# Kernel optimization log

Hardware: AMD Instinct MI355X
Metric: run time of the kernel (lower is better)

The kernel has to match this reference:

```python
import jax, jax.numpy as jnp
import numpy as np

STATE_LEN = 128
SEQ_LEN = 2048  # middle segment length; total T = SEQ_LEN + 2*STATE_LEN = 2304


def _l2norm(t):
    # matches torch F.normalize(p=2, dim=-1, eps=1e-12)
    n = jnp.sqrt(jnp.sum(t * t, axis=-1, keepdims=True))
    return t / jnp.maximum(n, 1e-12)


def setup_inputs() -> dict:
    key = jax.random.key(0)
    ks = jax.random.split(key, 8)
    B, D, H, dk, dv = 1, 1024, 16, 64, 64
    T = SEQ_LEN + 2 * STATE_LEN
    x = jax.random.normal(ks[0], (B, T, D), dtype=jnp.float32)
    w = lambda k, do: jax.random.normal(k, (H, D, do), dtype=jnp.float32) * 0.02
    return {
        "x": x,
        "Wq": w(ks[1], dk),
        "Wk": w(ks[2], dk),
        "Wv": w(ks[3], dv),
        "Wq_state": w(ks[4], dk),
        "Wk_state": w(ks[5], dk),
        "Wv_state": w(ks[6], dv),
        "scaling_factor": jnp.full((H,), 1.0 / np.sqrt(dk), dtype=jnp.float32),
    }


def reference(x, Wq, Wk, Wv, Wq_state, Wk_state, Wv_state, scaling_factor):
    sl, seq = STATE_LEN, SEQ_LEN
    # extract_state: [start_state | sequence | end_state]
    x0 = x[:, :sl]
    xm = x[:, sl:sl + seq]
    x1 = x[:, sl + seq:]

    proj = lambda t, W: jnp.einsum('bsd,hdk->bhsk', t, W)  # StackedLinear, no bias

    q = jnp.concatenate([_l2norm(proj(x0, Wq_state)), _l2norm(proj(xm, Wq)), _l2norm(proj(x1, Wq_state))], axis=2)
    k = jnp.concatenate([_l2norm(proj(x0, Wk_state)), _l2norm(proj(xm, Wk)), _l2norm(proj(x1, Wk_state))], axis=2)
    v = jnp.concatenate([_l2norm(proj(x0, Wv_state)), _l2norm(proj(xm, Wv)), _l2norm(proj(x1, Wv_state))], axis=2)

    T = q.shape[2]
    row = jnp.arange(T)[:, None]
    col = jnp.arange(T)[None, :]
    allowed = col <= row  # causal (tril, diagonal=0)
    # end-state rows may not attend to start-state cols (attn_bias[..., seq+sl:seq+2sl, :sl] = 0 before log)
    allowed = allowed & ~((row >= sl + seq) & (col < sl))
    mask = jnp.where(allowed, 0.0, -jnp.inf).astype(q.dtype)  # log of 0/1 tril

    # per-head learnable scale applied to q@k^T, then additive mask, softmax, @v
    scores = jnp.einsum('bhqd,bhkd->bhqk', q, k) * scaling_factor[None, :, None, None] + mask
    att = jax.nn.softmax(scores, axis=-1)
    return jnp.einsum('bhqk,bhkd->bhqd', att, v)
```

## Files before the change

kernel.cpp:

```cpp
#include <hip/hip_runtime.h>
#include <hip/hip_bf16.h>

#define T_TOT 2304
#define DDIM  1024
#define NH    16
#define DK    64
#define SLEN  128
#define SEQ   2048

typedef __bf16 bf16x8 __attribute__((ext_vector_type(8)));
typedef __bf16 bf16x4 __attribute__((ext_vector_type(4)));
typedef float  f32x4  __attribute__((ext_vector_type(4)));

__device__ __forceinline__ void async_copy16(const void* gsrc, void* ldst) {
  __builtin_amdgcn_global_load_lds(
      (const __attribute__((address_space(1))) void*)gsrc,
      (__attribute__((address_space(3))) void*)ldst, 16, 0, 0);
}

__global__ __launch_bounds__(256) void convert_kernel(
    const float* __restrict__ x,
    const float* __restrict__ Wq, const float* __restrict__ Wk,
    const float* __restrict__ Wv, const float* __restrict__ Wqs,
    const float* __restrict__ Wks, const float* __restrict__ Wvs,
    __bf16* __restrict__ xb, __bf16* __restrict__ Wt) {
  const int b = blockIdx.x;
  const int tid = threadIdx.x;
  if (b < 576) {
    const float4* xin = (const float4*)x;
#pragma unroll
    for (int it = 0; it < 4; ++it) {
      int idx4 = b * 1024 + it * 256 + tid;
      float4 v = xin[idx4];
      bf16x4 o;
      o[0] = (__bf16)v.x; o[1] = (__bf16)v.y; o[2] = (__bf16)v.z; o[3] = (__bf16)v.w;
      *(bf16x4*)(xb + (size_t)idx4 * 4) = o;
    }
    return;
  }
  __shared__ float tile[64 * 65];
  const int wb = b - 576;
  const int m  = wb >> 8;
  const int rem = wb & 255;
  const int h  = rem >> 4;
  const int dt = rem & 15;
  const int d0 = dt * 64;
  const float* Wsrc = (m == 0 ? Wq : m == 1 ? Wk : m == 2 ? Wv
                      : m == 3 ? Wqs : m == 4 ? Wks : Wvs) + (size_t)h * (DDIM * DK);
#pragma unroll
  for (int rr = 0; rr < 4; ++rr) {
    int drow = rr * 16 + (tid >> 4);
    int nc   = (tid & 15) * 4;
    float4 v = *(const float4*)(Wsrc + (size_t)(d0 + drow) * DK + nc);
    tile[(nc + 0) * 65 + drow] = v.x;
    tile[(nc + 1) * 65 + drow] = v.y;
    tile[(nc + 2) * 65 + drow] = v.z;
    tile[(nc + 3) * 65 + drow] = v.w;
  }
  __syncthreads();
  {
    int n  = tid >> 2;
    int rg = (tid & 3) * 16;
    __bf16* dst = Wt + (((size_t)(m * NH + h)) * DK + n) * DDIM + d0 + rg;
    bf16x8 o0, o1;
#pragma unroll
    for (int e = 0; e < 8; e++) o0[e] = (__bf16)tile[n * 65 + rg + e];
#pragma unroll
    for (int e = 0; e < 8; e++) o1[e] = (__bf16)tile[n * 65 + rg + 8 + e];
    *(bf16x8*)dst = o0;
    *(bf16x8*)(dst + 8) = o1;
  }
}

__global__ __launch_bounds__(256) void proj_kernel(
    const __bf16* __restrict__ xb, const __bf16* __restrict__ Wt,
    const float* __restrict__ scal,
    __bf16* __restrict__ qkv, __bf16* __restrict__ vt) {
  const int ntile = blockIdx.x;
  const int rt    = blockIdx.y;
  const int which = blockIdx.z;
  const int r0    = rt * 128;
  const int m     = (rt == 0 || rt == 17) ? which + 3 : which;

  __shared__ __bf16 Xs[128 * 64];
  __shared__ __bf16 Wsh[128 * 64];

  const int tid  = threadIdx.x;
  const int wave = tid >> 6, lane = tid & 63;
  const int quad = lane >> 4, lc = lane & 15;
  const int wr   = wave >> 1, wc = wave & 1;
  const int h    = ntile * 2 + wc;

  const __bf16* Wbase = Wt + ((size_t)m * NH) * (DK * DDIM) + (size_t)(ntile * 128) * DDIM;

  const f32x4 fz = {0.f, 0.f, 0.f, 0.f};
  f32x4 acc[4][4];
#pragma unroll
  for (int i = 0; i < 4; i++)
#pragma unroll
    for (int j = 0; j < 4; j++) acc[i][j] = fz;

  for (int k0 = 0; k0 < DDIM; k0 += 64) {
#pragma unroll
    for (int it = 0; it < 4; ++it) {
      int L = it * 256 + tid;
      int row = L >> 3, c = (L & 7) ^ ((L >> 3) & 7);
      async_copy16(xb + (size_t)(r0 + row) * DDIM + k0 + c * 8,
                   (char*)Xs + (size_t)(it * 256 + wave * 64) * 16);
    }
#pragma unroll
    for (int it = 0; it < 4; ++it) {
      int L = it * 256 + tid;
      int row = L >> 3, c = (L & 7) ^ ((L >> 3) & 7);
      async_copy16(Wbase + (size_t)row * DDIM + k0 + c * 8,
                   (char*)Wsh + (size_t)(it * 256 + wave * 64) * 16);
    }
    __syncthreads();
#pragma unroll
    for (int kk = 0; kk < 2; kk++) {
      bf16x8 afr[4], bfr[4];
#pragma unroll
      for (int i = 0; i < 4; i++) {
        int row = wr * 64 + i * 16 + lc;
        int ch  = (kk * 4 + quad) ^ (row & 7);
        afr[i] = *(const bf16x8*)(Xs + (row * 8 + ch) * 8);
      }
#pragma unroll
      for (int j = 0; j < 4; j++) {
        int row = wc * 64 + j * 16 + lc;
        int ch  = (kk * 4 + quad) ^ (row & 7);
        bfr[j] = *(const bf16x8*)(Wsh + (row * 8 + ch) * 8);
      }
#pragma unroll
      for (int i = 0; i < 4; i++)
#pragma unroll
        for (int j = 0; j < 4; j++)
          acc[i][j] = __builtin_amdgcn_mfma_f32_16x16x32_bf16(afr[i], bfr[j], acc[i][j], 0, 0, 0);
    }
    __syncthreads();
  }

  const float qscale = (which == 0) ? scal[h] : 1.0f;
  float inv4[4][4];
#pragma unroll
  for (int i = 0; i < 4; i++) {
#pragma unroll
    for (int r = 0; r < 4; r++) {
      float s = 0.f;
#pragma unroll
      for (int j = 0; j < 4; j++) { float v = acc[i][j][r]; s += v * v; }
#pragma unroll
      for (int off = 1; off < 16; off <<= 1) s += __shfl_xor(s, off, 64);
      inv4[i][r] = qscale / fmaxf(sqrtf(s), 1e-12f);
    }
  }
  if (which == 2) {
    __bf16* vtp = vt + (size_t)h * (DK * T_TOT);
#pragma unroll
    for (int i = 0; i < 4; i++) {
      int rowbase = r0 + wr * 64 + i * 16 + quad * 4;
#pragma unroll
      for (int j = 0; j < 4; j++) {
        bf16x4 o;
#pragma unroll
        for (int r = 0; r < 4; r++) o[r] = (__bf16)(acc[i][j][r] * inv4[i][r]);
        *(bf16x4*)(vtp + (size_t)(j * 16 + lc) * T_TOT + rowbase) = o;
      }
    }
  } else {
    __bf16* outp = qkv + ((size_t)(which * NH + h)) * ((size_t)T_TOT * DK);
#pragma unroll
    for (int i = 0; i < 4; i++)
#pragma unroll
      for (int r = 0; r < 4; r++) {
        int row = r0 + wr * 64 + i * 16 + quad * 4 + r;
#pragma unroll
        for (int j = 0; j < 4; j++)
          outp[(size_t)row * DK + j * 16 + lc] = (__bf16)(acc[i][j][r] * inv4[i][r]);
      }
  }
}

__global__ __launch_bounds__(256) void attn_kernel(
    const __bf16* __restrict__ qkv, const __bf16* __restrict__ vt,
    float* __restrict__ out) {
  const int b    = blockIdx.x;
  const int h    = b & 15;
  const int qg   = 35 - (b >> 4);
  const int q0b  = qg * 64;
  const int tid  = threadIdx.x;
  const int wave = tid >> 6, lane = tid & 63;
  const int quad = lane >> 4, lc = lane & 15;
  const int q0w  = q0b + wave * 16;

  const __bf16* qp = qkv + ((size_t)h) * ((size_t)T_TOT * DK);
  const __bf16* kp = qkv + ((size_t)(NH + h)) * ((size_t)T_TOT * DK);
  const __bf16* vp = vt + (size_t)h * (DK * T_TOT);

  __shared__ __bf16 Ks[2][64 * 64];
  __shared__ __bf16 Vs[2][64 * 64];
  __shared__ __bf16 Ps[4][16 * 64];

  bf16x8 qf[2];
#pragma unroll
  for (int kk = 0; kk < 2; kk++)
    qf[kk] = *(const bf16x8*)(qp + (size_t)(q0w + lc) * DK + kk * 32 + quad * 8);

  const f32x4 fz = {0.f, 0.f, 0.f, 0.f};
  f32x4 acc_o[4];
#pragma unroll
  for (int ct = 0; ct < 4; ct++) acc_o[ct] = fz;
  float m_i = -__builtin_inff(), l_i = 0.f;

  const int jstart = (q0b >= SLEN + SEQ) ? 2 : 0;
  const int jend   = qg;

  auto stage = [&](int j, int bufi) {
    const __bf16* kT = kp + (size_t)j * 64 * DK;
#pragma unroll
    for (int it = 0; it < 2; ++it) {
      int L = it * 256 + tid;
      int row = L >> 3, c = (L & 7) ^ (L >> 3 & 7);
      async_copy16(kT + row * DK + c * 8,
                   (char*)&Ks[bufi][0] + (size_t)(it * 256 + wave * 64) * 16);
    }
#pragma unroll
    for (int it = 0; it < 2; ++it) {
      int L = it * 256 + tid;
      int row = L >> 3, c = (L & 7) ^ (L >> 3 & 7);
      async_copy16(vp + (size_t)row * T_TOT + j * 64 + c * 8,
                   (char*)&Vs[bufi][0] + (size_t)(it * 256 + wave * 64) * 16);
    }
  };

  stage(jstart, 0);
  int cur = 0;

  for (int j = jstart; j <= jend; ++j) {
    __syncthreads();
    if (j < jend) stage(j + 1, cur ^ 1);

    const int c0 = j * 64;
    const bool diag = (j == jend);

    f32x4 s[4];
#pragma unroll
    for (int ct = 0; ct < 4; ct++) {
      s[ct] = fz;
#pragma unroll
      for (int kk = 0; kk < 2; kk++) {
        int row = ct * 16 + lc;
        bf16x8 kA = *(const bf16x8*)(&Ks[cur][(row * 8 + (((kk * 4 + quad)) ^ (row & 7))) * 8]);
        s[ct] = __builtin_amdgcn_mfma_f32_16x16x32_bf16(kA, qf[kk], s[ct], 0, 0, 0);
      }
    }

    float mx = -__builtin_inff();
#pragma unroll
    for (int ct = 0; ct < 4; ct++)
#pragma unroll
      for (int r = 0; r < 4; r++) {
        float v = s[ct][r];
        if (diag && (c0 + ct * 16 + quad * 4 + r) > (q0w + lc)) v = -__builtin_inff();
        s[ct][r] = v;
        mx = fmaxf(mx, v);
      }
    mx = fmaxf(mx, __shfl_xor(mx, 16, 64));
    mx = fmaxf(mx, __shfl_xor(mx, 32, 64));
    float mnew  = fmaxf(m_i, mx);
    float alpha = __expf(m_i - mnew);
    float rs = 0.f;
#pragma unroll
    for (int ct = 0; ct < 4; ct++)
#pragma unroll
      for (int r = 0; r < 4; r++) {
        float pe = __expf(s[ct][r] - mnew);
        s[ct][r] = pe;
        rs += pe;
      }
    rs += __shfl_xor(rs, 16, 64);
    rs += __shfl_xor(rs, 32, 64);
    l_i = l_i * alpha + rs;
    m_i = mnew;
#pragma unroll
    for (int ct = 0; ct < 4; ct++)
#pragma unroll
      for (int r = 0; r < 4; r++) acc_o[ct][r] *= alpha;

#pragma unroll
    for (int ct = 0; ct < 4; ct++) {
      bf16x4 pb;
#pragma unroll
      for (int r = 0; r < 4; r++) pb[r] = (__bf16)s[ct][r];
      int cc = ct * 2 + (quad >> 1);
      int el = lc * 64 + ((cc ^ (lc & 7)) * 8) + (quad & 1) * 4;
      *(bf16x4*)(&Ps[wave][el]) = pb;
    }

#pragma unroll
    for (int kq = 0; kq < 2; kq++) {
      int cc = kq * 4 + quad;
      bf16x8 pB = *(const bf16x8*)(&Ps[wave][lc * 64 + ((cc ^ (lc & 7)) * 8)]);
#pragma unroll
      for (int ct = 0; ct < 4; ct++) {
        int vrow = ct * 16 + lc;
        bf16x8 vA = *(const bf16x8*)(&Vs[cur][(vrow * 8 + ((cc) ^ (vrow & 7))) * 8]);
        acc_o[ct] = __builtin_amdgcn_mfma_f32_16x16x32_bf16(vA, pB, acc_o[ct], 0, 0, 0);
      }
    }
    cur ^= 1;
  }

  float invl = 1.0f / l_i;
#pragma unroll
  for (int ct = 0; ct < 4; ct++) {
    f32x4 o;
#pragma unroll
    for (int r = 0; r < 4; r++) o[r] = acc_o[ct][r] * invl;
    *(f32x4*)(&out[((size_t)h * T_TOT + q0w + lc) * DK + ct * 16 + quad * 4]) = o;
  }
}

extern "C" void kernel_launch(void* const* d_in, const int* in_sizes, int n_in,
                              void* d_out, int out_size, void* d_ws, size_t ws_size,
                              hipStream_t stream) {
  const float* x    = (const float*)d_in[0];
  const float* Wq   = (const float*)d_in[1];
  const float* Wk   = (const float*)d_in[2];
  const float* Wv   = (const float*)d_in[3];
  const float* Wqs  = (const float*)d_in[4];
  const float* Wks  = (const float*)d_in[5];
  const float* Wvs  = (const float*)d_in[6];
  const float* scal = (const float*)d_in[7];
  float* out = (float*)d_out;

  char* ws = (char*)d_ws;
  size_t off = 0;
  __bf16* xb  = (__bf16*)(ws + off); off += (size_t)T_TOT * DDIM * 2;
  __bf16* Wt  = (__bf16*)(ws + off); off += (size_t)6 * NH * DK * DDIM * 2;
  __bf16* qkv = (__bf16*)(ws + off); off += (size_t)2 * NH * T_TOT * DK * 2;
  __bf16* vt  = (__bf16*)(ws + off);

  convert_kernel<<<2112, 256, 0, stream>>>(x, Wq, Wk, Wv, Wqs, Wks, Wvs, xb, Wt);
  proj_kernel<<<dim3(8, 18, 3), 256, 0, stream>>>(xb, Wt, scal, qkv, vt);
  attn_kernel<<<dim3(576), 256, 0, stream>>>(qkv, vt, out);
}
```

Before: 163.8 us.

## Use 128-wide KV tiles in attention and fold log2e into query scale

The attention loop now stages 128-key K and V tiles per iteration instead of 64, with a 16-chunk XOR swizzle for V and P. This halves the number of loop iterations and barriers per query block, and on the diagonal tile it skips the MFMAs that would be fully masked. The query scale is premultiplied by log2(e) so the softmax can use exp2f in place of __expf. Shared memory per block doubles and register pressure rises, which may reduce occupancy.

```diff
diff --git a/kernel.cpp b/kernel.cpp
--- a/kernel.cpp
+++ b/kernel.cpp
@@ -140,7 +140,7 @@
     __syncthreads();
   }
 
-  const float qscale = (which == 0) ? scal[h] : 1.0f;
+  const float qscale = (which == 0) ? scal[h] * 1.44269504088896f : 1.0f;
   float inv4[4][4];
 #pragma unroll
   for (int i = 0; i < 4; i++) {
@@ -197,9 +197,9 @@
   const __bf16* kp = qkv + ((size_t)(NH + h)) * ((size_t)T_TOT * DK);
   const __bf16* vp = vt + (size_t)h * (DK * T_TOT);
 
-  __shared__ __bf16 Ks[2][64 * 64];
-  __shared__ __bf16 Vs[2][64 * 64];
-  __shared__ __bf16 Ps[4][16 * 64];
+  __shared__ __bf16 Ks[2][128 * 64];
+  __shared__ __bf16 Vs[2][64 * 128];
+  __shared__ __bf16 Ps[4][16 * 128];
 
   bf16x8 qf[2];
 #pragma unroll
@@ -212,23 +212,23 @@
   for (int ct = 0; ct < 4; ct++) acc_o[ct] = fz;
   float m_i = -__builtin_inff(), l_i = 0.f;
 
-  const int jstart = (q0b >= SLEN + SEQ) ? 2 : 0;
-  const int jend   = qg;
+  const int jstart = (q0b >= SLEN + SEQ) ? 1 : 0;
+  const int jend   = q0b >> 7;
 
   auto stage = [&](int j, int bufi) {
-    const __bf16* kT = kp + (size_t)j * 64 * DK;
-#pragma unroll
-    for (int it = 0; it < 2; ++it) {
+    const __bf16* kT = kp + (size_t)j * 128 * DK;
+#pragma unroll
+    for (int it = 0; it < 4; ++it) {
       int L = it * 256 + tid;
-      int row = L >> 3, c = (L & 7) ^ (L >> 3 & 7);
+      int row = L >> 3, c = (L & 7) ^ ((L >> 3) & 7);
       async_copy16(kT + row * DK + c * 8,
                    (char*)&Ks[bufi][0] + (size_t)(it * 256 + wave * 64) * 16);
     }
 #pragma unroll
-    for (int it = 0; it < 2; ++it) {
+    for (int it = 0; it < 4; ++it) {
       int L = it * 256 + tid;
-      int row = L >> 3, c = (L & 7) ^ (L >> 3 & 7);
-      async_copy16(vp + (size_t)row * T_TOT + j * 64 + c * 8,
+      int d = L >> 4, c = (L & 15) ^ ((L >> 4) & 15);
+      async_copy16(vp + (size_t)d * T_TOT + j * 128 + c * 8,
                    (char*)&Vs[bufi][0] + (size_t)(it * 256 + wave * 64) * 16);
     }
   };
@@ -240,44 +240,58 @@
     __syncthreads();
     if (j < jend) stage(j + 1, cur ^ 1);
 
-    const int c0 = j * 64;
+    const int c0 = j * 128;
     const bool diag = (j == jend);
-
-    f32x4 s[4];
-#pragma unroll
-    for (int ct = 0; ct < 4; ct++) {
+    const int ctmax = diag ? ((q0b & 64) ? 7 : 3) : 7;
+
+    f32x4 s[8];
+#pragma unroll
+    for (int ct = 0; ct < 8; ct++) {
       s[ct] = fz;
-#pragma unroll
-      for (int kk = 0; kk < 2; kk++) {
-        int row = ct * 16 + lc;
-        bf16x8 kA = *(const bf16x8*)(&Ks[cur][(row * 8 + (((kk * 4 + quad)) ^ (row & 7))) * 8]);
-        s[ct] = __builtin_amdgcn_mfma_f32_16x16x32_bf16(kA, qf[kk], s[ct], 0, 0, 0);
+      if (ct <= ctmax) {
+#pragma unroll
+        for (int kk = 0; kk < 2; kk++) {
+          int row = ct * 16 + lc;
+          bf16x8 kA = *(const bf16x8*)(&Ks[cur][(row * 8 + ((kk * 4 + quad) ^ (row & 7))) * 8]);
+          s[ct] = __builtin_amdgcn_mfma_f32_16x16x32_bf16(kA, qf[kk], s[ct], 0, 0, 0);
+        }
       }
     }
 
     float mx = -__builtin_inff();
-#pragma unroll
-    for (int ct = 0; ct < 4; ct++)
-#pragma unroll
-      for (int r = 0; r < 4; r++) {
-        float v = s[ct][r];
-        if (diag && (c0 + ct * 16 + quad * 4 + r) > (q0w + lc)) v = -__builtin_inff();
-        s[ct][r] = v;
-        mx = fmaxf(mx, v);
-      }
+    if (diag) {
+#pragma unroll
+      for (int ct = 0; ct < 8; ct++) {
+        if (ct > ctmax) break;
+#pragma unroll
+        for (int r = 0; r < 4; r++) {
+          float v = s[ct][r];
+          if ((c0 + ct * 16 + quad * 4 + r) > (q0w + lc)) v = -__builtin_inff();
+          s[ct][r] = v;
+          mx = fmaxf(mx, v);
+        }
+      }
+    } else {
+#pragma unroll
+      for (int ct = 0; ct < 8; ct++)
+#pragma unroll
+        for (int r = 0; r < 4; r++) mx = fmaxf(mx, s[ct][r]);
+    }
     mx = fmaxf(mx, __shfl_xor(mx, 16, 64));
     mx = fmaxf(mx, __shfl_xor(mx, 32, 64));
     float mnew  = fmaxf(m_i, mx);
-    float alpha = __expf(m_i - mnew);
+    float alpha = exp2f(m_i - mnew);
     float rs = 0.f;
 #pragma unroll
-    for (int ct = 0; ct < 4; ct++)
+    for (int ct = 0; ct < 8; ct++) {
+      if (ct > ctmax) break;
 #pragma unroll
       for (int r = 0; r < 4; r++) {
-        float pe = __expf(s[ct][r] - mnew);
+        float pe = exp2f(s[ct][r] - mnew);
         s[ct][r] = pe;
         rs += pe;
       }
+    }
     rs += __shfl_xor(rs, 16, 64);
     rs += __shfl_xor(rs, 32, 64);
     l_i = l_i * alpha + rs;
@@ -288,23 +302,26 @@
       for (int r = 0; r < 4; r++) acc_o[ct][r] *= alpha;
 
 #pragma unroll
-    for (int ct = 0; ct < 4; ct++) {
+    for (int ct = 0; ct < 8; ct++) {
+      if (ct > ctmax) break;
       bf16x4 pb;
 #pragma unroll
       for (int r = 0; r < 4; r++) pb[r] = (__bf16)s[ct][r];
       int cc = ct * 2 + (quad >> 1);
-      int el = lc * 64 + ((cc ^ (lc & 7)) * 8) + (quad & 1) * 4;
+      int el = lc * 128 + ((cc ^ (lc & 15)) * 8) + (quad & 1) * 4;
       *(bf16x4*)(&Ps[wave][el]) = pb;
     }
 
-#pragma unroll
-    for (int kq = 0; kq < 2; kq++) {
+    const int kqmax = diag ? ((q0b & 64) ? 3 : 1) : 3;
+#pragma unroll
+    for (int kq = 0; kq < 4; kq++) {
+      if (kq > kqmax) break;
       int cc = kq * 4 + quad;
-      bf16x8 pB = *(const bf16x8*)(&Ps[wave][lc * 64 + ((cc ^ (lc & 7)) * 8)]);
+      bf16x8 pB = *(const bf16x8*)(&Ps[wave][lc * 128 + ((cc ^ (lc & 15)) * 8)]);
 #pragma unroll
       for (int ct = 0; ct < 4; ct++) {
-        int vrow = ct * 16 + lc;
-        bf16x8 vA = *(const bf16x8*)(&Vs[cur][(vrow * 8 + ((cc) ^ (vrow & 7))) * 8]);
+        int d = ct * 16 + lc;
+        bf16x8 vA = *(const bf16x8*)(&Vs[cur][(d * 16 + (cc ^ (d & 15))) * 8]);
         acc_o[ct] = __builtin_amdgcn_mfma_f32_16x16x32_bf16(vA, pB, acc_o[ct], 0, 0, 0);
       }
     }
```

Result: faster. 157.5 us (-3.9%).
